# Performance work log

Hardware: AMD Instinct MI355X
Metric: run time of the kernel (lower is better)

## Reference

```python
import jax, jax.numpy as jnp
import numpy as np

N, C, P, M = 8, 20, 8732, 16
THRESHOLD, NEG_POS_RATIO, ALPHA = 0.5, 3, 1.0


def cxcy_to_xy(c):
    return jnp.concatenate([c[..., :2] - c[..., 2:] / 2.0, c[..., :2] + c[..., 2:] / 2.0], axis=-1)


def xy_to_cxcy(xy):
    return jnp.concatenate([(xy[..., :2] + xy[..., 2:]) / 2.0, xy[..., 2:] - xy[..., :2]], axis=-1)


def cxcy_to_gcxgcy(cxcy, priors):
    g_cxcy = (cxcy[..., :2] - priors[..., :2]) / (priors[..., 2:] / 10.0)
    g_wh = jnp.log(cxcy[..., 2:] / priors[..., 2:]) * 5.0
    return jnp.concatenate([g_cxcy, g_wh], axis=-1)


def jaccard(a, b):
    # a: (M,4), b: (P,4), boundary coords -> IoU (M,P)
    lo = jnp.maximum(a[:, None, :2], b[None, :, :2])
    hi = jnp.minimum(a[:, None, 2:], b[None, :, 2:])
    inter = jnp.prod(jnp.clip(hi - lo, 0.0), axis=-1)
    area_a = jnp.prod(a[:, 2:] - a[:, :2], axis=-1)
    area_b = jnp.prod(b[:, 2:] - b[:, :2], axis=-1)
    return inter / (area_a[:, None] + area_b[None, :] - inter)


def setup_inputs() -> dict:
    key = jax.random.key(0)
    k1, k2, k3, k4, k5, k6 = jax.random.split(key, 6)
    predicted_locs = jax.random.normal(k1, (N, C, P, 4), jnp.float32)
    predicted_scores = jax.random.normal(k2, (N, C, P, 2), jnp.float32)
    # valid ground-truth boundary boxes (x1<x2, y1<y2) in [0,1]
    ctr = jax.random.uniform(k3, (N, C, M, 2), minval=0.2, maxval=0.8)
    wh = jax.random.uniform(k4, (N, C, M, 2), minval=0.05, maxval=0.3)
    boxes = jnp.concatenate([ctr - wh / 2.0, ctr + wh / 2.0], axis=-1)
    # valid priors in cxcywh (w,h > 0 so log-encoding is finite)
    pctr = jax.random.uniform(k5, (P, 2), minval=0.05, maxval=0.95)
    pwh = jax.random.uniform(k6, (P, 2), minval=0.05, maxval=0.5)
    priors_cxcy = jnp.concatenate([pctr, pwh], axis=-1)
    labels = jnp.ones((N, C, M), jnp.int32)  # binary per-class head: object label = 1
    return {
        "predicted_locs": predicted_locs,
        "predicted_scores": predicted_scores,
        "boxes": boxes,
        "labels": labels,
        "priors_cxcy": priors_cxcy,
    }


def _forward(predicted_locs, predicted_scores, boxes, priors_cxcy, labels):
    n_classes = predicted_scores.shape[1]
    n_priors = predicted_scores.shape[2]
    priors_xy = cxcy_to_xy(priors_cxcy)

    def match(b, lab):
        # b: (M,4) boundary, lab: (M,) int
        ov = jaccard(b, priors_xy)                       # (M,P)
        obj_for_prior = jnp.argmax(ov, axis=0)           # (P,)
        ov_for_prior = jnp.max(ov, axis=0)               # (P,)
        prior_for_obj = jnp.argmax(ov, axis=1)           # (M,)
        # force each object to own its best prior
        obj_for_prior = obj_for_prior.at[prior_for_obj].set(jnp.arange(b.shape[0]))
        ov_for_prior = ov_for_prior.at[prior_for_obj].set(1.0)
        cls = jnp.where(ov_for_prior < THRESHOLD, 0, lab[obj_for_prior])  # (P,)
        tl = cxcy_to_gcxgcy(xy_to_cxcy(b[obj_for_prior]), priors_cxcy)    # (P,4)
        return tl, cls

    true_locs, true_classes = jax.vmap(jax.vmap(match))(boxes, labels)  # (N,C,P,4), (N,C,P)

    pos = true_classes != 0                      # (N,C,P)
    posf = pos.astype(predicted_locs.dtype)
    n_pos_bc = posf.sum(axis=2)                  # (N,C) positives per image per class
    n_pos_c = n_pos_bc.sum(axis=0)               # (C,)

    # localization: mean L1 over positive priors (4 coords each), per class
    l1 = jnp.abs(predicted_locs - true_locs).sum(-1) * posf   # (N,C,P)
    loc_loss_c = l1.sum(axis=(0, 2)) / jnp.maximum(n_pos_c * 4.0, 1.0)

    # per-prior binary cross entropy
    logp = jax.nn.log_softmax(predicted_scores, axis=-1)      # (N,C,P,2)
    ce = -jnp.take_along_axis(logp, true_classes[..., None], axis=-1)[..., 0]  # (N,C,P)
    conf_pos_c = (ce * posf).sum(axis=(0, 2))

    # hard negative mining: sort negatives desc per (image,class) row, keep top 3*n_pos
    ce_neg = jnp.where(pos, 0.0, ce)
    ce_neg_sorted = -jnp.sort(-ce_neg, axis=-1)               # (N,C,P) descending
    n_hard = NEG_POS_RATIO * n_pos_bc                         # (N,C)
    ranks = jnp.arange(n_priors, dtype=n_hard.dtype)
    hard_mask = ranks[None, None, :] < n_hard[..., None]
    conf_hard_c = (ce_neg_sorted * hard_mask).sum(axis=(0, 2))

    safe = jnp.maximum(n_pos_c, 1.0)
    loss_c = jnp.where(
        n_pos_c > 0,
        (conf_pos_c + conf_hard_c + ALPHA * loc_loss_c) / safe,
        0.0,
    ) / n_classes
    return loss_c.sum()


def reference(predicted_locs, predicted_scores, boxes, labels, priors_cxcy):
    return _forward(predicted_locs, predicted_scores, boxes, priors_cxcy, labels)
```

## Files before the change

### kernel.cpp

```cpp
#include <hip/hip_runtime.h>
#include <math.h>

#define NN 8
#define CC 20
#define PP 8732
#define MM 16
#define NPR 3
#define ROWS (NN * CC)
#define FBLK 1024
#define EPT 9

__device__ __forceinline__ float fast_rcp(float x) { return __builtin_amdgcn_rcpf(x); }
__device__ __forceinline__ float rfl(float x) {
    return __uint_as_float(__builtin_amdgcn_readfirstlane(__float_as_uint(x)));
}

__device__ __forceinline__ float lse2(float a, float b) {
    float mx = fmaxf(a, b);
    float d  = fabsf(a - b);
    return mx + __logf(1.0f + __expf(-d));
}

__global__ __launch_bounds__(FBLK) void mbox_fused(
    const float* __restrict__ locs, const float* __restrict__ scores,
    const float* __restrict__ boxes, const int* __restrict__ labels,
    const float* __restrict__ priors, float* __restrict__ rstats)
{
    const int row = blockIdx.x, tid = threadIdx.x, lane = tid & 63, wav = tid >> 6;

    __shared__ unsigned int s_u32[PP];
    __shared__ unsigned char s_pkb[PP];
    __shared__ unsigned long long s_pk64[16 * MM];
    __shared__ float s_bcx[MM], s_bcy[MM], s_bw[MM], s_bh[MM];
    __shared__ float s_rf[16 * 3];
    __shared__ int s_lab[MM], s_pfo[MM];
    __shared__ unsigned int s_hist[256];
    __shared__ unsigned int s_prefix, s_Kr, s_K;
    __shared__ float s_redf[16];
    __shared__ int s_redi[16];

    const float* bb = boxes + (size_t)row * MM * 4;
    unsigned int labm = 0;
    {
        const int* lb = labels + (size_t)row * MM;
#pragma unroll
        for (int m = 0; m < MM; m++) labm |= (lb[m] != 0 ? 1u : 0u) << m;
        labm = __builtin_amdgcn_readfirstlane(labm);
    }
    if (tid < MM) {
        const float* b = bb + tid * 4;
        float x1 = b[0], y1 = b[1], x2 = b[2], y2 = b[3];
        s_bcx[tid] = (x1 + x2) * 0.5f;
        s_bcy[tid] = (y1 + y2) * 0.5f;
        s_bw[tid]  = x2 - x1;
        s_bh[tid]  = y2 - y1;
        s_lab[tid] = labels[row * MM + tid];
    }
    __syncthreads();

    const float4* pri4 = (const float4*)priors;
    const float4* loc4 = (const float4*)(locs + (size_t)row * PP * 4);
    const float2* sc2  = (const float2*)(scores + (size_t)row * PP * 2);

#pragma unroll
    for (int pass4 = 0; pass4 < 4; pass4++) {
        const int m0 = pass4 * 4;
        float x1[4], y1[4], x2[4], y2[4], ar[4];
#pragma unroll
        for (int m = 0; m < 4; m++) {
            float a1 = rfl(bb[(m0 + m) * 4 + 0]), b1 = rfl(bb[(m0 + m) * 4 + 1]);
            float a2 = rfl(bb[(m0 + m) * 4 + 2]), b2 = rfl(bb[(m0 + m) * 4 + 3]);
            x1[m] = a1; y1[m] = b1; x2[m] = a2; y2[m] = b2;
            ar[m] = rfl((a2 - a1) * (b2 - b1));
        }
        unsigned int bestk4[4];
#pragma unroll
        for (int m = 0; m < 4; m++) bestk4[m] = 0u;

#pragma unroll
        for (int k = 0; k < EPT; k++) {
            const int p = tid + k * FBLK;
            if (p >= PP) continue;
            float4 pr = pri4[p];
            const unsigned int lowb = (unsigned int)(8 - k);
            float hw = pr.z * 0.5f, hh = pr.w * 0.5f;
            float px1 = pr.x - hw, py1 = pr.y - hh;
            float px2 = pr.x + hw, py2 = pr.y + hh;
            float area_b = (px2 - px1) * (py2 - py1);
            unsigned int bv = (pass4 == 0) ? 0u : s_u32[p];
#pragma unroll
            for (int m = 0; m < 4; m++) {
                float dx = fminf(x2[m], px2) - fmaxf(x1[m], px1);
                float dy = fminf(y2[m], py2) - fmaxf(y1[m], py1);
                dx = fmaxf(dx, 0.0f); dy = fmaxf(dy, 0.0f);
                float inter = dx * dy;
                float den = (ar[m] + area_b) - inter;
                float iou = inter * fast_rcp(den);
                unsigned int ib = __float_as_uint(iou);
                bv        = max(bv,        (ib & 0xFFFFFFF0u) | (unsigned int)(15 - (m0 + m)));
                bestk4[m] = max(bestk4[m], (ib & 0xFFFFFFF0u) | lowb);
            }
            s_u32[p] = bv;
        }

#pragma unroll
        for (int m = 0; m < 4; m++) {
            unsigned int bk = bestk4[m];
            int kk = 8 - (int)(bk & 0xFu);
            int pb = tid + kk * FBLK;
            unsigned long long key = ((unsigned long long)(bk & 0xFFFFFFF0u) << 32)
                                   | (unsigned int)(0x7fffffff - pb);
#pragma unroll
            for (int off = 32; off; off >>= 1) {
                unsigned long long o = __shfl_down(key, off);
                if (o > key) key = o;
            }
            if (lane == 0) s_pk64[wav * MM + m0 + m] = key;
        }
        __builtin_amdgcn_sched_barrier(0);
    }

    float l_np = 0.0f, l_l1 = 0.0f, l_cp = 0.0f;
#pragma unroll
    for (int k = 0; k < EPT; k++) {
        const int p = tid + k * FBLK;
        if (p >= PP) continue;
        unsigned int bv = s_u32[p];
        int bm = 15 - (int)(bv & 15u);
        bool pos = (bv >= 0x3F000000u) && (((labm >> bm) & 1u) != 0u);
        s_pkb[p] = (unsigned char)((pos ? 16u : 0u) | (unsigned)bm);
        float2 sc = sc2[p];
        float lse = lse2(sc.x, sc.y);
        if (pos) {
            float4 pr = pri4[p];
            float4 pl = loc4[p];
            l_np += 1.0f;
            l_cp += lse - sc.y;
            float tx = (s_bcx[bm] - pr.x) * 10.0f / pr.z;
            float ty = (s_bcy[bm] - pr.y) * 10.0f / pr.w;
            float tw = __logf(s_bw[bm] / pr.z) * 5.0f;
            float th = __logf(s_bh[bm] / pr.w) * 5.0f;
            l_l1 += fabsf(pl.x - tx) + fabsf(pl.y - ty) + fabsf(pl.z - tw) + fabsf(pl.w - th);
            s_u32[p] = 0u;
        } else {
            s_u32[p] = __float_as_uint(fmaxf(lse - sc.x, 0.0f));
        }
    }

#pragma unroll
    for (int off = 32; off; off >>= 1) {
        l_np += __shfl_down(l_np, off);
        l_l1 += __shfl_down(l_l1, off);
        l_cp += __shfl_down(l_cp, off);
    }
    if (lane == 0) { s_rf[wav * 3] = l_np; s_rf[wav * 3 + 1] = l_l1; s_rf[wav * 3 + 2] = l_cp; }
    __syncthreads();

    if (tid < MM) {
        unsigned long long key = s_pk64[tid];
        for (int w = 1; w < 16; w++) {
            unsigned long long o = s_pk64[w * MM + tid];
            if (o > key) key = o;
        }
        s_pfo[tid] = 0x7fffffff - (int)(unsigned)(key & 0xffffffffull);
    }
    __syncthreads();

    float d_np = 0, d_l1 = 0, d_cp = 0;
    if (tid < MM) {
        int p = s_pfo[tid];
        bool is_last = true;
        for (int mm = tid + 1; mm < MM; mm++) if (s_pfo[mm] == p) is_last = false;
        if (is_last) {
            const float4 pr = ((const float4*)priors)[p];
            const float4 pl = loc4[p];
            const float2 sc = sc2[p];
            float lse = lse2(sc.x, sc.y);
            unsigned int u = s_pkb[p];
            if (u & 16u) {
                int mo = u & 15;
                d_np -= 1.0f; d_cp -= (lse - sc.y);
                float tx = (s_bcx[mo] - pr.x) * 10.0f / pr.z;
                float ty = (s_bcy[mo] - pr.y) * 10.0f / pr.w;
                float tw = __logf(s_bw[mo] / pr.z) * 5.0f;
                float th = __logf(s_bh[mo] / pr.w) * 5.0f;
                d_l1 -= fabsf(pl.x - tx) + fabsf(pl.y - ty) + fabsf(pl.z - tw) + fabsf(pl.w - th);
            }
            if (s_lab[tid] != 0) {
                d_np += 1.0f; d_cp += (lse - sc.y);
                float tx = (s_bcx[tid] - pr.x) * 10.0f / pr.z;
                float ty = (s_bcy[tid] - pr.y) * 10.0f / pr.w;
                float tw = __logf(s_bw[tid] / pr.z) * 5.0f;
                float th = __logf(s_bh[tid] / pr.w) * 5.0f;
                d_l1 += fabsf(pl.x - tx) + fabsf(pl.y - ty) + fabsf(pl.z - tw) + fabsf(pl.w - th);
                s_u32[p] = 0u;
            } else {
                s_u32[p] = __float_as_uint(fmaxf(lse - sc.x, 0.0f));
            }
        }
    }
    if (tid < 64) {
#pragma unroll
        for (int off = 32; off; off >>= 1) {
            d_np += __shfl_down(d_np, off);
            d_l1 += __shfl_down(d_l1, off);
            d_cp += __shfl_down(d_cp, off);
        }
        if (tid == 0) {
            float np0 = 0, l10 = 0, cp0 = 0;
            for (int w = 0; w < 16; w++) {
                np0 += s_rf[w * 3]; l10 += s_rf[w * 3 + 1]; cp0 += s_rf[w * 3 + 2];
            }
            float np = np0 + d_np;
            rstats[(size_t)row * 8 + 0] = np;
            rstats[(size_t)row * 8 + 1] = l10 + d_l1;
            rstats[(size_t)row * 8 + 2] = cp0 + d_cp;
            int K = NPR * (int)(np + 0.5f);
            s_K = (K > 0) ? (unsigned)K : 0u;
            s_prefix = 0u;
            s_Kr = (K > 0) ? (unsigned)K : 0u;
        }
    }
    __syncthreads();

    const unsigned int K = s_K;
    unsigned int T = 0u;
    if (K > 0u && K < PP) {
        for (int pass = 0; pass < 4; pass++) {
            const int shift = 24 - 8 * pass;
            if (tid < 256) s_hist[tid] = 0u;
            __syncthreads();
            const unsigned int pref   = s_prefix;
            const unsigned int maskhi = (pass == 0) ? 0u : (0xffffffffu << (shift + 8));
#pragma unroll
            for (int k = 0; k < EPT; k++) {
                const int p = tid + k * FBLK;
                unsigned int u = (p < PP) ? s_u32[p] : 0u;
                if ((u & maskhi) == pref) atomicAdd(&s_hist[(u >> shift) & 255u], 1u);
            }
            __syncthreads();
            if (wav == 0) {
                unsigned int Kr = s_Kr;
                unsigned int h0 = s_hist[lane * 4 + 0];
                unsigned int h1 = s_hist[lane * 4 + 1];
                unsigned int h2 = s_hist[lane * 4 + 2];
                unsigned int h3 = s_hist[lane * 4 + 3];
                unsigned int c3 = h3;
                unsigned int c2 = h3 + h2;
                unsigned int c1 = c2 + h1;
                unsigned int c0 = c1 + h0;
                unsigned int suf = c0;
#pragma unroll
                for (int off = 1; off < 64; off <<= 1) {
                    unsigned int o = __shfl_down(suf, off);
                    if (lane + off < 64) suf += o;
                }
                unsigned int above = suf - c0;
                int cand = -1;
                unsigned int G = 0;
                if      (c3 + above >= Kr) { cand = lane * 4 + 3; G = above + c3 - h3; }
                else if (c2 + above >= Kr) { cand = lane * 4 + 2; G = above + c2 - h2; }
                else if (c1 + above >= Kr) { cand = lane * 4 + 1; G = above + c1 - h1; }
                else if (c0 + above >= Kr) { cand = lane * 4 + 0; G = above + c0 - h0; }
                int best = cand;
#pragma unroll
                for (int off = 32; off; off >>= 1) best = max(best, __shfl_down(best, off));
                best = __shfl(best, 0);
                if (cand == best && cand >= 0) {
                    s_Kr = Kr - G;
                    s_prefix = pref | ((unsigned int)best << shift);
                }
            }
            __syncthreads();
        }
        T = s_prefix;
    }

    float sgt = 0.0f; int cgt = 0;
    if (K > 0u) {
#pragma unroll
        for (int k = 0; k < EPT; k++) {
            const int p = tid + k * FBLK;
            unsigned int u = (p < PP) ? s_u32[p] : 0u;
            if (u > T) { sgt += __uint_as_float(u); cgt++; }
        }
    }
#pragma unroll
    for (int off = 32; off; off >>= 1) {
        sgt += __shfl_down(sgt, off);
        cgt += __shfl_down(cgt, off);
    }
    if (lane == 0) { s_redf[wav] = sgt; s_redi[wav] = cgt; }
    __syncthreads();
    if (tid == 0) {
        float s = 0; int cnt = 0;
        for (int w = 0; w < 16; w++) { s += s_redf[w]; cnt += s_redi[w]; }
        float chard = (K > 0u) ? (s + (float)(int)(K - (unsigned)cnt) * __uint_as_float(T)) : 0.0f;
        rstats[(size_t)row * 8 + 4] = chard;
    }
}

__global__ void mbox_finalize(const float* __restrict__ rstats, float* __restrict__ out) {
    int c = threadIdx.x;
    float loss = 0.0f;
    if (c < CC) {
        float np = 0, l1 = 0, cp = 0, ch = 0;
        for (int n = 0; n < NN; n++) {
            const float* s = rstats + ((size_t)(n * CC + c)) * 8;
            np += s[0]; l1 += s[1]; cp += s[2]; ch += s[4];
        }
        float loc = l1 / fmaxf(np * 4.0f, 1.0f);
        float val = (np > 0.0f) ? (cp + ch + loc) / fmaxf(np, 1.0f) : 0.0f;
        loss = val / (float)CC;
    }
#pragma unroll
    for (int off = 32; off; off >>= 1) loss += __shfl_down(loss, off);
    if (threadIdx.x == 0) out[0] = loss;
}

extern "C" void kernel_launch(void* const* d_in, const int* in_sizes, int n_in,
                              void* d_out, int out_size, void* d_ws, size_t ws_size,
                              hipStream_t stream) {
    const float* locs   = (const float*)d_in[0];
    const float* scores = (const float*)d_in[1];
    const float* boxes  = (const float*)d_in[2];
    const int*   labels = (const int*)d_in[3];
    const float* priors = (const float*)d_in[4];
    float* out = (float*)d_out;

    float* rstats = (float*)d_ws;

    mbox_fused<<<ROWS, FBLK, 0, stream>>>(locs, scores, boxes, labels, priors, rstats);
    mbox_finalize<<<1, 64, 0, stream>>>(rstats, out);
}
```

Baseline: 121.6 us.

## Split prior matching across multiple blocks per row, then select in second kernel

Breaks the per-row fused kernel into a matching kernel that runs 8 smaller 256-thread blocks per row over chunks of priors, writing per-prior CE values, packed match bytes, per-chunk best-prior keys and partial stats to workspace. A second kernel per row merges the partial keys, reloads CE into LDS, applies the forced-match correction and does the radix top-K selection. The aim is to raise occupancy and parallelism in the IoU phase, which previously used only 160 large blocks. The cost is extra global round-trips through workspace and an additional kernel launch.

```diff
diff --git a/kernel.cpp b/kernel.cpp
--- a/kernel.cpp
+++ b/kernel.cpp
@@ -7,6 +7,12 @@
 #define MM 16
 #define NPR 3
 #define ROWS (NN * CC)
+
+#define SPL 8
+#define CH2 1092
+#define TBA 256
+#define KA 5
+
 #define FBLK 1024
 #define EPT 9
 
@@ -21,23 +27,22 @@
     return mx + __logf(1.0f + __expf(-d));
 }
 
-__global__ __launch_bounds__(FBLK) void mbox_fused(
+__global__ __launch_bounds__(TBA) void mbox_match(
     const float* __restrict__ locs, const float* __restrict__ scores,
     const float* __restrict__ boxes, const int* __restrict__ labels,
-    const float* __restrict__ priors, float* __restrict__ rstats)
+    const float* __restrict__ priors,
+    float* __restrict__ cef, unsigned char* __restrict__ pk8,
+    unsigned long long* __restrict__ partials, float* __restrict__ cstats)
 {
-    const int row = blockIdx.x, tid = threadIdx.x, lane = tid & 63, wav = tid >> 6;
-
-    __shared__ unsigned int s_u32[PP];
-    __shared__ unsigned char s_pkb[PP];
-    __shared__ unsigned long long s_pk64[16 * MM];
+    const int row = blockIdx.x / SPL;
+    const int chunk = blockIdx.x - row * SPL;
+    const int tid = threadIdx.x, lane = tid & 63, wav = tid >> 6;
+    const int p0 = chunk * CH2, p1e = min(p0 + CH2, PP);
+
+    __shared__ unsigned int s_u32[CH2];
+    __shared__ unsigned long long s_pk64[4 * MM];
     __shared__ float s_bcx[MM], s_bcy[MM], s_bw[MM], s_bh[MM];
-    __shared__ float s_rf[16 * 3];
-    __shared__ int s_lab[MM], s_pfo[MM];
-    __shared__ unsigned int s_hist[256];
-    __shared__ unsigned int s_prefix, s_Kr, s_K;
-    __shared__ float s_redf[16];
-    __shared__ int s_redi[16];
+    __shared__ float s_rf[4 * 3];
 
     const float* bb = boxes + (size_t)row * MM * 4;
     unsigned int labm = 0;
@@ -54,7 +59,6 @@
         s_bcy[tid] = (y1 + y2) * 0.5f;
         s_bw[tid]  = x2 - x1;
         s_bh[tid]  = y2 - y1;
-        s_lab[tid] = labels[row * MM + tid];
     }
     __syncthreads();
 
@@ -78,16 +82,16 @@
         for (int m = 0; m < 4; m++) bestk4[m] = 0u;
 
 #pragma unroll
-        for (int k = 0; k < EPT; k++) {
-            const int p = tid + k * FBLK;
-            if (p >= PP) continue;
+        for (int k = 0; k < KA; k++) {
+            const int p = p0 + tid + k * TBA;
+            if (p >= p1e) continue;
             float4 pr = pri4[p];
             const unsigned int lowb = (unsigned int)(8 - k);
             float hw = pr.z * 0.5f, hh = pr.w * 0.5f;
             float px1 = pr.x - hw, py1 = pr.y - hh;
             float px2 = pr.x + hw, py2 = pr.y + hh;
             float area_b = (px2 - px1) * (py2 - py1);
-            unsigned int bv = (pass4 == 0) ? 0u : s_u32[p];
+            unsigned int bv = (pass4 == 0) ? 0u : s_u32[tid + k * TBA];
 #pragma unroll
             for (int m = 0; m < 4; m++) {
                 float dx = fminf(x2[m], px2) - fmaxf(x1[m], px1);
@@ -100,14 +104,14 @@
                 bv        = max(bv,        (ib & 0xFFFFFFF0u) | (unsigned int)(15 - (m0 + m)));
                 bestk4[m] = max(bestk4[m], (ib & 0xFFFFFFF0u) | lowb);
             }
-            s_u32[p] = bv;
+            s_u32[tid + k * TBA] = bv;
         }
 
 #pragma unroll
         for (int m = 0; m < 4; m++) {
             unsigned int bk = bestk4[m];
             int kk = 8 - (int)(bk & 0xFu);
-            int pb = tid + kk * FBLK;
+            int pb = p0 + tid + kk * TBA;
             unsigned long long key = ((unsigned long long)(bk & 0xFFFFFFF0u) << 32)
                                    | (unsigned int)(0x7fffffff - pb);
 #pragma unroll
@@ -122,15 +126,16 @@
 
     float l_np = 0.0f, l_l1 = 0.0f, l_cp = 0.0f;
 #pragma unroll
-    for (int k = 0; k < EPT; k++) {
-        const int p = tid + k * FBLK;
-        if (p >= PP) continue;
-        unsigned int bv = s_u32[p];
+    for (int k = 0; k < KA; k++) {
+        const int p = p0 + tid + k * TBA;
+        if (p >= p1e) continue;
+        unsigned int bv = s_u32[tid + k * TBA];
         int bm = 15 - (int)(bv & 15u);
         bool pos = (bv >= 0x3F000000u) && (((labm >> bm) & 1u) != 0u);
-        s_pkb[p] = (unsigned char)((pos ? 16u : 0u) | (unsigned)bm);
+        pk8[(size_t)row * PP + p] = (unsigned char)((pos ? 16u : 0u) | (unsigned)bm);
         float2 sc = sc2[p];
         float lse = lse2(sc.x, sc.y);
+        float ce;
         if (pos) {
             float4 pr = pri4[p];
             float4 pl = loc4[p];
@@ -141,10 +146,11 @@
             float tw = __logf(s_bw[bm] / pr.z) * 5.0f;
             float th = __logf(s_bh[bm] / pr.w) * 5.0f;
             l_l1 += fabsf(pl.x - tx) + fabsf(pl.y - ty) + fabsf(pl.z - tw) + fabsf(pl.w - th);
-            s_u32[p] = 0u;
+            ce = 0.0f;
         } else {
-            s_u32[p] = __float_as_uint(fmaxf(lse - sc.x, 0.0f));
-        }
+            ce = fmaxf(lse - sc.x, 0.0f);
+        }
+        cef[(size_t)row * PP + p] = ce;
     }
 
 #pragma unroll
@@ -158,14 +164,64 @@
 
     if (tid < MM) {
         unsigned long long key = s_pk64[tid];
-        for (int w = 1; w < 16; w++) {
+        for (int w = 1; w < 4; w++) {
             unsigned long long o = s_pk64[w * MM + tid];
             if (o > key) key = o;
         }
+        partials[((size_t)row * MM + tid) * SPL + chunk] = key;
+    }
+    if (tid == 0) {
+        float np = 0, l1 = 0, cp = 0;
+        for (int w = 0; w < 4; w++) { np += s_rf[w * 3]; l1 += s_rf[w * 3 + 1]; cp += s_rf[w * 3 + 2]; }
+        float* cs = cstats + ((size_t)row * SPL + chunk) * 3;
+        cs[0] = np; cs[1] = l1; cs[2] = cp;
+    }
+}
+
+__global__ __launch_bounds__(FBLK) void mbox_sel(
+    const float* __restrict__ locs, const float* __restrict__ scores,
+    const float* __restrict__ boxes, const int* __restrict__ labels,
+    const float* __restrict__ priors,
+    const float* __restrict__ cef, const unsigned char* __restrict__ pk8,
+    const unsigned long long* __restrict__ partials,
+    const float* __restrict__ cstats, float* __restrict__ rstats)
+{
+    const int row = blockIdx.x, tid = threadIdx.x, lane = tid & 63, wav = tid >> 6;
+
+    __shared__ unsigned int s_u32[PP];
+    __shared__ float s_bcx[MM], s_bcy[MM], s_bw[MM], s_bh[MM];
+    __shared__ int s_lab[MM], s_pfo[MM];
+    __shared__ float s_sum[3];
+    __shared__ unsigned int s_hist[256];
+    __shared__ unsigned int s_prefix, s_Kr, s_K;
+    __shared__ float s_redf[16];
+    __shared__ int s_redi[16];
+
+    if (tid < MM) {
+        const float* b = boxes + ((size_t)row * MM + tid) * 4;
+        float x1 = b[0], y1 = b[1], x2 = b[2], y2 = b[3];
+        s_bcx[tid] = (x1 + x2) * 0.5f; s_bcy[tid] = (y1 + y2) * 0.5f;
+        s_bw[tid] = x2 - x1; s_bh[tid] = y2 - y1;
+        s_lab[tid] = labels[row * MM + tid];
+        const unsigned long long* pr = partials + ((size_t)row * MM + tid) * SPL;
+        unsigned long long key = pr[0];
+        for (int c = 1; c < SPL; c++) { unsigned long long o = pr[c]; if (o > key) key = o; }
         s_pfo[tid] = 0x7fffffff - (int)(unsigned)(key & 0xffffffffull);
     }
-    __syncthreads();
-
+    if (tid >= 16 && tid < 19) {
+        int j = tid - 16; float s = 0;
+        for (int c = 0; c < SPL; c++) s += cstats[((size_t)row * SPL + c) * 3 + j];
+        s_sum[j] = s;
+    }
+#pragma unroll
+    for (int k = 0; k < EPT; k++) {
+        const int p = tid + k * FBLK;
+        if (p < PP) s_u32[p] = __float_as_uint(cef[(size_t)row * PP + p]);
+    }
+    __syncthreads();
+
+    const float4* loc4 = (const float4*)(locs + (size_t)row * PP * 4);
+    const float2* sc2  = (const float2*)(scores + (size_t)row * PP * 2);
     float d_np = 0, d_l1 = 0, d_cp = 0;
     if (tid < MM) {
         int p = s_pfo[tid];
@@ -176,7 +232,7 @@
             const float4 pl = loc4[p];
             const float2 sc = sc2[p];
             float lse = lse2(sc.x, sc.y);
-            unsigned int u = s_pkb[p];
+            unsigned int u = pk8[(size_t)row * PP + p];
             if (u & 16u) {
                 int mo = u & 15;
                 d_np -= 1.0f; d_cp -= (lse - sc.y);
@@ -207,14 +263,10 @@
             d_cp += __shfl_down(d_cp, off);
         }
         if (tid == 0) {
-            float np0 = 0, l10 = 0, cp0 = 0;
-            for (int w = 0; w < 16; w++) {
-                np0 += s_rf[w * 3]; l10 += s_rf[w * 3 + 1]; cp0 += s_rf[w * 3 + 2];
-            }
-            float np = np0 + d_np;
+            float np = s_sum[0] + d_np;
             rstats[(size_t)row * 8 + 0] = np;
-            rstats[(size_t)row * 8 + 1] = l10 + d_l1;
-            rstats[(size_t)row * 8 + 2] = cp0 + d_cp;
+            rstats[(size_t)row * 8 + 1] = s_sum[1] + d_l1;
+            rstats[(size_t)row * 8 + 2] = s_sum[2] + d_cp;
             int K = NPR * (int)(np + 0.5f);
             s_K = (K > 0) ? (unsigned)K : 0u;
             s_prefix = 0u;
@@ -328,8 +380,16 @@
     const float* priors = (const float*)d_in[4];
     float* out = (float*)d_out;
 
-    float* rstats = (float*)d_ws;
-
-    mbox_fused<<<ROWS, FBLK, 0, stream>>>(locs, scores, boxes, labels, priors, rstats);
+    char* ws = (char*)d_ws;
+    float* cef                   = (float*)ws;
+    unsigned char* pk8           = (unsigned char*)(ws + 5588480);
+    unsigned long long* partials = (unsigned long long*)(ws + 6985600);
+    float* cstats                = (float*)(ws + 7149440);
+    float* rstats                = (float*)(ws + 7164800);
+
+    mbox_match<<<ROWS * SPL, TBA, 0, stream>>>(locs, scores, boxes, labels, priors,
+                                               cef, pk8, partials, cstats);
+    mbox_sel<<<ROWS, FBLK, 0, stream>>>(locs, scores, boxes, labels, priors,
+                                        cef, pk8, partials, cstats, rstats);
     mbox_finalize<<<1, 64, 0, stream>>>(rstats, out);
 }
```

Result: no change. 122.1 us (+0.4%).
